# Performance work log

Hardware: AMD Instinct MI355X
Metric: run time of the kernel (lower is better)

Reference implementation:

```python
import jax, jax.numpy as jnp
import numpy as np

VOCAB, EMBED, CONV_C, HID, LABELS = 50257, 512, 512, 1024, 128
B, S = 32, 1024

def setup_inputs() -> dict:
    key = jax.random.key(0)
    ks = jax.random.split(key, 8)
    sc = lambda d: 1.0 / np.sqrt(d)
    return {
        "token_ids": jax.random.randint(ks[0], (B, S), 0, VOCAB),
        "emb_table": jax.random.normal(ks[1], (VOCAB, EMBED), jnp.float32) * 0.02,
        "conv_w": jax.random.normal(ks[2], (CONV_C, EMBED), jnp.float32) * sc(EMBED),
        "conv_b": jnp.zeros((CONV_C,), jnp.float32),
        "dec_w1": jax.random.normal(ks[3], (CONV_C, HID), jnp.float32) * sc(CONV_C),
        "dec_b1": jnp.zeros((HID,), jnp.float32),
        "dec_w2": jax.random.normal(ks[4], (HID, LABELS), jnp.float32) * sc(HID),
        "dec_b2": jnp.zeros((LABELS,), jnp.float32),
    }

def reference(token_ids, emb_table, conv_w, conv_b, dec_w1, dec_b1, dec_w2, dec_b2):
    # Embedding lookup: [B, S, E]
    x = emb_table[token_ids]
    # DocNN encoder on a length-1 sequence = kernel-1 conv + relu (+ trivial max-over-time)
    h = jax.nn.relu(jnp.einsum('bse,ce->bsc', x, conv_w) + conv_b)  # [B,S,C]
    # MLP decoder per word
    z = jax.nn.relu(jnp.einsum('bsc,ch->bsh', h, dec_w1) + dec_b1)  # [B,S,H]
    logits = jnp.einsum('bsh,hl->bsl', z, dec_w2) + dec_b2          # [B,S,L]
    # torch.cat over dim 0 of per-word outputs -> flat [B*S, L]
    return logits.reshape(-1, logits.shape[-1])
```

## Files before the change

kernel.cpp:

```cpp
#include <hip/hip_runtime.h>

typedef __bf16 bf16;
typedef __bf16 bf16x4 __attribute__((ext_vector_type(4)));
typedef __bf16 bf16x8 __attribute__((ext_vector_type(8)));
typedef float f32x4 __attribute__((ext_vector_type(4)));

#define NROWS 32768
#define EMBED 512
#define CONV_C 512
#define HID 1024
#define LABELS 128

__device__ inline void async16(const void* g, void* l) {
  __builtin_amdgcn_global_load_lds(
      (const __attribute__((address_space(1))) void*)g,
      (__attribute__((address_space(3))) void*)l, 16, 0, 0);
}

__device__ inline int bitswap02(int g) {
  return ((g & 1) << 2) | (g & 0xA) | ((g >> 2) & 1);
}

__device__ inline bf16x8 cvt8_sw(const float* row, int o0, int o1) {
  f32x4 lo = *(const f32x4*)(row + o0);
  f32x4 hi = *(const f32x4*)(row + o1);
  bf16x8 r;
  r[0] = (bf16)lo[0]; r[1] = (bf16)lo[1]; r[2] = (bf16)lo[2]; r[3] = (bf16)lo[3];
  r[4] = (bf16)hi[0]; r[5] = (bf16)hi[1]; r[6] = (bf16)hi[2]; r[7] = (bf16)hi[3];
  return r;
}


__global__ void cvt_bf16(const float* __restrict__ in, bf16* __restrict__ out, int n) {
  int i = (blockIdx.x * blockDim.x + threadIdx.x) * 4;
  if (i >= n) return;
  float4 v = *(const float4*)(in + i);
  bf16x4 o;
  o.x = (bf16)v.x; o.y = (bf16)v.y; o.z = (bf16)v.z; o.w = (bf16)v.w;
  *(bf16x4*)(out + i) = o;
}

__global__ void transpose_cvt(const float* __restrict__ in, bf16* __restrict__ out,
                              int K, int N) {
  __shared__ float t[64][65];
  int kb = blockIdx.x * 64, nb = blockIdx.y * 64;
  for (int i = threadIdx.x; i < 4096; i += 256) {
    int r = i >> 6, c = i & 63;
    t[r][c] = in[(size_t)(kb + r) * N + nb + c];
  }
  __syncthreads();
  for (int i = threadIdx.x; i < 4096; i += 256) {
    int r = i >> 6, c = i & 63;
    out[(size_t)(nb + r) * K + kb + c] = (bf16)t[c][r];
  }
}

__global__ __launch_bounds__(512, 2) void gemm1_gather(
    const int* __restrict__ tok, const float* __restrict__ emb,
    const bf16* __restrict__ convw, const float* __restrict__ bias,
    bf16* __restrict__ out, int M, int N, int K) {
  __shared__ __attribute__((aligned(16))) char smem[131072];
  const int tid = threadIdx.x, wave = tid >> 6, lane = tid & 63;
  const int m0 = blockIdx.x * 128;
  const int am0 = (wave >> 2) * 64;
  const int bn0 = (wave & 3) * 64;
  const int lrow = lane & 15, quad = lane >> 4;

  int a_r[4], a_c[4];
#pragma unroll
  for (int c = 0; c < 4; ++c) {
    int s = tid + c * 512;
    int r = s >> 4, p = s & 15;
    a_r[c] = r;
    a_c[c] = ((((p & 7) ^ (r & 7)) | (p & 8))) * 4;
  }
  int trow[4];
#pragma unroll
  for (int c = 0; c < 4; ++c) trow[c] = tok[m0 + a_r[c]];

  int b_r[4], b_c[4];
#pragma unroll
  for (int c = 0; c < 4; ++c) {
    int s = tid + c * 512;
    b_r[c] = s >> 3;
    b_c[c] = ((s & 7) ^ (b_r[c] & 7)) * 8;
  }

  auto stageA = [&](int p, int k0) {
    float* lAf = (float*)(smem + p * 32768);
#pragma unroll
    for (int c = 0; c < 4; ++c)
      async16(emb + (size_t)trow[c] * EMBED + k0 + a_c[c],
              lAf + (size_t)(tid + c * 512) * 4);
  };
  auto stageB = [&](int p, int cn0, int k0) {
    bf16* lB = (bf16*)(smem + 65536 + p * 32768);
#pragma unroll
    for (int c = 0; c < 4; ++c)
      async16(convw + (size_t)(cn0 + b_r[c]) * EMBED + k0 + b_c[c],
              lB + (size_t)(tid + c * 512) * 8);
  };

  const f32x4 zero4 = {0.f, 0.f, 0.f, 0.f};

  for (int chunk = 0; chunk < 2; ++chunk) {
    const int cn0 = chunk * 256;
    stageA(0, 0);
    stageB(0, cn0, 0);

    f32x4 acc[4][4];
#pragma unroll
    for (int i = 0; i < 4; ++i)
#pragma unroll
      for (int j = 0; j < 4; ++j) acc[i][j] = zero4;

    int cur = 0;
    for (int it = 0; it < 8; ++it) {
      __syncthreads();
      if (it < 7) {
        stageA(cur ^ 1, (it + 1) * 64);
        stageB(cur ^ 1, cn0, (it + 1) * 64);
      }
      const float* lAf = (const float*)(smem + cur * 32768);
      const bf16* lB = (const bf16*)(smem + 65536 + cur * 32768);
#pragma unroll
      for (int ks = 0; ks < 2; ++ks) {
        bf16x8 a[4], b[4];
#pragma unroll
        for (int t = 0; t < 4; ++t) {
          int r = am0 + t * 16 + lrow, sw = r & 7;
          int p0 = ks * 8 + ((2 * quad) ^ sw);
          int p1 = ks * 8 + ((2 * quad + 1) ^ sw);
          a[t] = cvt8_sw(lAf + r * 64, p0 * 4, p1 * 4);
        }
#pragma unroll
        for (int t = 0; t < 4; ++t) {
          int rn = bn0 + t * 16 + lrow;
          b[t] = *(const bf16x8*)(lB + rn * 64 + (((ks * 4 + quad) ^ (rn & 7)) * 8));
        }
#pragma unroll
        for (int mi = 0; mi < 4; ++mi)
#pragma unroll
          for (int ni = 0; ni < 4; ++ni)
            acc[mi][ni] =
                __builtin_amdgcn_mfma_f32_16x16x32_bf16(a[mi], b[ni], acc[mi][ni], 0, 0, 0);
      }
      cur ^= 1;
    }

#pragma unroll
    for (int mi = 0; mi < 4; ++mi) {
#pragma unroll
      for (int ni = 0; ni < 4; ++ni) {
        int col = cn0 + bn0 + ni * 16 + lrow;
        float bv = bias[col];
#pragma unroll
        for (int r = 0; r < 4; ++r) {
          int row = m0 + am0 + mi * 16 + quad * 4 + r;
          float v = acc[mi][ni][r] + bv;
          v = v > 0.f ? v : 0.f;
          out[(size_t)row * CONV_C + col] = (bf16)v;
        }
      }
    }
  }
}

__global__ __launch_bounds__(512, 2) void gemm23_fused(
    const bf16* __restrict__ h,
    const bf16* __restrict__ w1t,
    const bf16* __restrict__ w2t,
    const float* __restrict__ b1, const float* __restrict__ b2,
    float* __restrict__ out) {
  __shared__ __attribute__((aligned(16))) char smem[131072];
  bf16* zbuf = (bf16*)(smem + 32768);
  const int tid = threadIdx.x, wave = tid >> 6, lane = tid & 63;
  const int m0 = blockIdx.x * 128;
  const int am0 = (wave >> 2) * 64;
  const int bn0 = (wave & 3) * 64;
  const int lb0 = (wave & 3) * 32;
  const int lrow = lane & 15, quad = lane >> 4;
  const int lsw = lrow & 7;
  const int bsw = bitswap02(lsw);

  int a_r[2], a_c[2];
#pragma unroll
  for (int c = 0; c < 2; ++c) {
    int s = tid + c * 512;
    a_r[c] = s >> 3;
    a_c[c] = ((s & 7) ^ (a_r[c] & 7)) * 8;
  }
  int b_r[4], b_c[4];
#pragma unroll
  for (int c = 0; c < 4; ++c) {
    int s = tid + c * 512;
    b_r[c] = s >> 3;
    b_c[c] = ((s & 7) ^ (b_r[c] & 7)) * 8;
  }
  int q_r[2], q_c[2];
#pragma unroll
  for (int c = 0; c < 2; ++c) {
    int s = tid + c * 512;
    q_r[c] = s >> 3;
    q_c[c] = ((s & 7) ^ (q_r[c] & 7)) * 8;
  }

  auto stageA = [&](int p, int k0) {
    bf16* lA = (bf16*)(smem + p * 16384);
#pragma unroll
    for (int c = 0; c < 2; ++c)
      async16(h + (size_t)(m0 + a_r[c]) * 512 + k0 + a_c[c],
              lA + (size_t)(tid + c * 512) * 8);
  };
  auto stageB = [&](int p, int cn0, int k0) {
    bf16* lB = (bf16*)(smem + 32768 + p * 32768);
#pragma unroll
    for (int c = 0; c < 4; ++c)
      async16(w1t + (size_t)(cn0 + b_r[c]) * 512 + k0 + b_c[c],
              lB + (size_t)(tid + c * 512) * 8);
  };
  auto stageQ = [&](int cn0, int qq, int pq) {
    bf16* lQ = (bf16*)(smem + 98304 + pq * 16384);
#pragma unroll
    for (int c = 0; c < 2; ++c)
      async16(w2t + (size_t)q_r[c] * HID + cn0 + qq * 64 + q_c[c],
              lQ + (size_t)(tid + c * 512) * 8);
  };

  const f32x4 zero4 = {0.f, 0.f, 0.f, 0.f};
  f32x4 out_acc[4][2];
#pragma unroll
  for (int i = 0; i < 4; ++i)
#pragma unroll
    for (int j = 0; j < 2; ++j) out_acc[i][j] = zero4;

  auto layer3 = [&](int qq, int pq) {
    const bf16* lQ = (const bf16*)(smem + 98304 + pq * 16384);
#pragma unroll
    for (int ks = 0; ks < 2; ++ks) {
      bf16x8 a3[4], b3[2];
#pragma unroll
      for (int t = 0; t < 4; ++t) {
        int m = am0 + t * 16 + lrow;
        int kq = qq * 8 + ks * 4 + quad;
        a3[t] = *(const bf16x8*)(zbuf + m * 256 + ((kq ^ bsw) << 3));
      }
#pragma unroll
      for (int t = 0; t < 2; ++t) {
        int lab = lb0 + t * 16 + lrow;
        b3[t] = *(const bf16x8*)(lQ + lab * 64 + (((ks * 4 + quad) ^ lsw) * 8));
      }
#pragma unroll
      for (int mi = 0; mi < 4; ++mi)
#pragma unroll
        for (int ni = 0; ni < 2; ++ni)
          out_acc[mi][ni] =
              __builtin_amdgcn_mfma_f32_16x16x32_bf16(a3[mi], b3[ni], out_acc[mi][ni], 0, 0, 0);
    }
  };

  for (int chunk = 0; chunk < 4; ++chunk) {
    const int cn0 = chunk * 256;
    if (chunk == 0) stageA(0, 0);
    stageB(0, cn0, 0);
    stageQ(cn0, 0, 0);

    f32x4 z_acc[4][4];
#pragma unroll
    for (int i = 0; i < 4; ++i)
#pragma unroll
      for (int j = 0; j < 4; ++j) z_acc[i][j] = zero4;

    int cur = 0;
    for (int it = 0; it < 8; ++it) {
      __syncthreads();
      if (it < 7) {
        stageB(cur ^ 1, cn0, (it + 1) * 64);
        stageA(cur ^ 1, (it + 1) * 64);
      }
      const bf16* lA = (const bf16*)(smem + cur * 16384);
      const bf16* lB = (const bf16*)(smem + 32768 + cur * 32768);
#pragma unroll
      for (int ks = 0; ks < 2; ++ks) {
        bf16x8 a[4], b[4];
#pragma unroll
        for (int t = 0; t < 4; ++t)
          a[t] = *(const bf16x8*)(lA + (am0 + t * 16 + lrow) * 64 +
                                  (((ks * 4 + quad) ^ lsw) * 8));
#pragma unroll
        for (int t = 0; t < 4; ++t)
          b[t] = *(const bf16x8*)(lB + (bn0 + t * 16 + lrow) * 64 +
                                  (((ks * 4 + quad) ^ lsw) * 8));
#pragma unroll
        for (int mi = 0; mi < 4; ++mi)
#pragma unroll
          for (int ni = 0; ni < 4; ++ni)
            z_acc[mi][ni] =
                __builtin_amdgcn_mfma_f32_16x16x32_bf16(a[mi], b[ni], z_acc[mi][ni], 0, 0, 0);
      }
      cur ^= 1;
    }

    __syncthreads();
    stageQ(cn0, 1, 1);
#pragma unroll
    for (int mi = 0; mi < 4; ++mi) {
#pragma unroll
      for (int ni = 0; ni < 4; ++ni) {
        int zcol = bn0 + ni * 16 + lrow;
        float bv = b1[cn0 + zcol];
        int q5 = zcol >> 3;
#pragma unroll
        for (int r = 0; r < 4; ++r) {
          int zrow = am0 + mi * 16 + quad * 4 + r;
          float v = z_acc[mi][ni][r] + bv;
          v = v > 0.f ? v : 0.f;
          zbuf[zrow * 256 + ((q5 ^ bitswap02(zrow & 7)) << 3) + (zcol & 7)] = (bf16)v;
        }
      }
    }
    __syncthreads();
    layer3(0, 0);
    __syncthreads();
    stageQ(cn0, 2, 0);
    layer3(1, 1);
    __syncthreads();
    stageQ(cn0, 3, 1);
    if (chunk < 3) stageA(0, 0);
    layer3(2, 0);
    __syncthreads();
    layer3(3, 1);
    __syncthreads();
  }

#pragma unroll
  for (int mi = 0; mi < 4; ++mi) {
#pragma unroll
    for (int ni = 0; ni < 2; ++ni) {
      int col = lb0 + ni * 16 + lrow;
      float bv = b2[col];
#pragma unroll
      for (int r = 0; r < 4; ++r) {
        int row = m0 + am0 + mi * 16 + quad * 4 + r;
        out[(size_t)row * LABELS + col] = out_acc[mi][ni][r] + bv;
      }
    }
  }
}


extern "C" void kernel_launch(void* const* d_in, const int* in_sizes, int n_in,
                              void* d_out, int out_size, void* d_ws, size_t ws_size,
                              hipStream_t stream) {
  const int* tok = (const int*)d_in[0];
  const float* emb = (const float*)d_in[1];
  const float* conv_w = (const float*)d_in[2];
  const float* conv_b = (const float*)d_in[3];
  const float* w1 = (const float*)d_in[4];
  const float* b1 = (const float*)d_in[5];
  const float* w2 = (const float*)d_in[6];
  const float* b2 = (const float*)d_in[7];
  float* out = (float*)d_out;

  char* ws = (char*)d_ws;
  bf16* wtc = (bf16*)(ws);
  bf16* wt1 = (bf16*)(ws + (1u << 19));
  bf16* wt2 = (bf16*)(ws + 3 * (1u << 19));
  bf16* h = (bf16*)(ws + (2u << 20));

  hipLaunchKernelGGL(cvt_bf16, dim3(256), dim3(256), 0, stream,
                     conv_w, wtc, CONV_C * EMBED);
  hipLaunchKernelGGL(transpose_cvt, dim3(8, 16), dim3(256), 0, stream,
                     w1, wt1, CONV_C, HID);
  hipLaunchKernelGGL(transpose_cvt, dim3(16, 2), dim3(256), 0, stream,
                     w2, wt2, HID, LABELS);

  hipLaunchKernelGGL(gemm1_gather, dim3(NROWS / 128), dim3(512),
                     0, stream, tok, emb, wtc, conv_b, h, NROWS, CONV_C, EMBED);
  hipLaunchKernelGGL(gemm23_fused, dim3(NROWS / 128), dim3(512),
                     0, stream, h, wt1, wt2, b1, b2, out);
}
```

Measured before the change: 237.1 us.

## Switch both GEMM mainloops to 4-stage, 32-wide K pipelines with explicit vmcnt waits

Both the gather GEMM and the fused layer-2 GEMM drop their double-buffered 64-wide K tiles for a ring of four 32-wide K slices, issued three slices ahead. Waits use explicit s_waitcnt vmcnt counts and raw s_barrier with sched_barrier fences, and the MFMA block is raised in priority with s_setprio. This aims to hide global-to-LDS latency better and to cut the full __syncthreads drains. In exchange there are twice as many barriers per K step, and the hand-tuned vmcnt counts are fragile; a wrong count is a silent race.

```diff
diff --git a/kernel.cpp b/kernel.cpp
--- a/kernel.cpp
+++ b/kernel.cpp
@@ -10,6 +10,14 @@
 #define CONV_C 512
 #define HID 1024
 #define LABELS 128
+
+#define VMCNT(n) asm volatile("s_waitcnt vmcnt(" #n ")" ::: "memory")
+
+__device__ inline void sbar() {
+  __builtin_amdgcn_sched_barrier(0);
+  __builtin_amdgcn_s_barrier();
+  __builtin_amdgcn_sched_barrier(0);
+}
 
 __device__ inline void async16(const void* g, void* l) {
   __builtin_amdgcn_global_load_lds(
@@ -66,47 +74,46 @@
   const int bn0 = (wave & 3) * 64;
   const int lrow = lane & 15, quad = lane >> 4;
 
-  int a_r[4], a_c[4];
-#pragma unroll
-  for (int c = 0; c < 4; ++c) {
+  int a_r[2], a_c[2];
+#pragma unroll
+  for (int c = 0; c < 2; ++c) {
     int s = tid + c * 512;
-    int r = s >> 4, p = s & 15;
-    a_r[c] = r;
-    a_c[c] = ((((p & 7) ^ (r & 7)) | (p & 8))) * 4;
-  }
-  int trow[4];
-#pragma unroll
-  for (int c = 0; c < 4; ++c) trow[c] = tok[m0 + a_r[c]];
-
-  int b_r[4], b_c[4];
-#pragma unroll
-  for (int c = 0; c < 4; ++c) {
+    a_r[c] = s >> 3;
+    a_c[c] = ((s & 7) ^ (a_r[c] & 7)) * 4;
+  }
+  int trow[2];
+#pragma unroll
+  for (int c = 0; c < 2; ++c) trow[c] = tok[m0 + a_r[c]];
+
+  int b_r[2], b_c[2];
+#pragma unroll
+  for (int c = 0; c < 2; ++c) {
     int s = tid + c * 512;
-    b_r[c] = s >> 3;
-    b_c[c] = ((s & 7) ^ (b_r[c] & 7)) * 8;
-  }
-
-  auto stageA = [&](int p, int k0) {
-    float* lAf = (float*)(smem + p * 32768);
-#pragma unroll
-    for (int c = 0; c < 4; ++c)
-      async16(emb + (size_t)trow[c] * EMBED + k0 + a_c[c],
-              lAf + (size_t)(tid + c * 512) * 4);
-  };
-  auto stageB = [&](int p, int cn0, int k0) {
-    bf16* lB = (bf16*)(smem + 65536 + p * 32768);
-#pragma unroll
-    for (int c = 0; c < 4; ++c)
-      async16(convw + (size_t)(cn0 + b_r[c]) * EMBED + k0 + b_c[c],
-              lB + (size_t)(tid + c * 512) * 8);
-  };
+    b_r[c] = s >> 2;
+    b_c[c] = ((s & 3) ^ (b_r[c] & 3)) * 8;
+  }
+
+  const int pA0 = (2 * quad) ^ (lrow & 7);
+  const int fswB = (quad ^ (lrow & 3)) << 3;
 
   const f32x4 zero4 = {0.f, 0.f, 0.f, 0.f};
 
   for (int chunk = 0; chunk < 2; ++chunk) {
     const int cn0 = chunk * 256;
-    stageA(0, 0);
-    stageB(0, cn0, 0);
+
+    auto stage_half = [&](int hh) {
+      const int sl = hh & 3, k0 = hh * 32;
+      float* lAf = (float*)(smem + sl * 16384);
+#pragma unroll
+      for (int c = 0; c < 2; ++c)
+        async16(emb + (size_t)trow[c] * EMBED + k0 + a_c[c],
+                lAf + (size_t)(tid + c * 512) * 4);
+      bf16* lB = (bf16*)(smem + 65536 + sl * 16384);
+#pragma unroll
+      for (int c = 0; c < 2; ++c)
+        async16(convw + (size_t)(cn0 + b_r[c]) * EMBED + k0 + b_c[c],
+                lB + (size_t)(tid + c * 512) * 8);
+    };
 
     f32x4 acc[4][4];
 #pragma unroll
@@ -114,38 +121,40 @@
 #pragma unroll
       for (int j = 0; j < 4; ++j) acc[i][j] = zero4;
 
-    int cur = 0;
-    for (int it = 0; it < 8; ++it) {
-      __syncthreads();
-      if (it < 7) {
-        stageA(cur ^ 1, (it + 1) * 64);
-        stageB(cur ^ 1, cn0, (it + 1) * 64);
-      }
-      const float* lAf = (const float*)(smem + cur * 32768);
-      const bf16* lB = (const bf16*)(smem + 65536 + cur * 32768);
-#pragma unroll
-      for (int ks = 0; ks < 2; ++ks) {
-        bf16x8 a[4], b[4];
-#pragma unroll
-        for (int t = 0; t < 4; ++t) {
-          int r = am0 + t * 16 + lrow, sw = r & 7;
-          int p0 = ks * 8 + ((2 * quad) ^ sw);
-          int p1 = ks * 8 + ((2 * quad + 1) ^ sw);
-          a[t] = cvt8_sw(lAf + r * 64, p0 * 4, p1 * 4);
-        }
-#pragma unroll
-        for (int t = 0; t < 4; ++t) {
-          int rn = bn0 + t * 16 + lrow;
-          b[t] = *(const bf16x8*)(lB + rn * 64 + (((ks * 4 + quad) ^ (rn & 7)) * 8));
-        }
-#pragma unroll
-        for (int mi = 0; mi < 4; ++mi)
-#pragma unroll
-          for (int ni = 0; ni < 4; ++ni)
-            acc[mi][ni] =
-                __builtin_amdgcn_mfma_f32_16x16x32_bf16(a[mi], b[ni], acc[mi][ni], 0, 0, 0);
-      }
-      cur ^= 1;
+    __builtin_amdgcn_sched_barrier(0);
+    stage_half(0); stage_half(1); stage_half(2);
+    VMCNT(8);
+    sbar();
+
+#pragma unroll
+    for (int hh = 0; hh < 16; ++hh) {
+      const float* lAf = (const float*)(smem + (hh & 3) * 16384);
+      const bf16* lB = (const bf16*)(smem + 65536 + (hh & 3) * 16384);
+      bf16x8 a[4], b[4];
+#pragma unroll
+      for (int t = 0; t < 4; ++t) {
+        int r = am0 + t * 16 + lrow;
+        a[t] = cvt8_sw(lAf + r * 32, pA0 * 4, (pA0 ^ 1) * 4);
+      }
+#pragma unroll
+      for (int t = 0; t < 4; ++t) {
+        int r = bn0 + t * 16 + lrow;
+        b[t] = *(const bf16x8*)(lB + r * 32 + fswB);
+      }
+      if (hh + 3 < 16) stage_half(hh + 3);
+      if (hh <= 12) { VMCNT(8); }
+      else if (hh == 13) { VMCNT(4); }
+      else { VMCNT(0); }
+      sbar();
+      __builtin_amdgcn_s_setprio(1);
+#pragma unroll
+      for (int mi = 0; mi < 4; ++mi)
+#pragma unroll
+        for (int ni = 0; ni < 4; ++ni)
+          acc[mi][ni] =
+              __builtin_amdgcn_mfma_f32_16x16x32_bf16(a[mi], b[ni], acc[mi][ni], 0, 0, 0);
+      __builtin_amdgcn_s_setprio(0);
+      sbar();
     }
 
 #pragma unroll
@@ -183,19 +192,14 @@
   const int lsw = lrow & 7;
   const int bsw = bitswap02(lsw);
 
-  int a_r[2], a_c[2];
+  const int a_r = tid >> 2;
+  const int a_c = ((tid & 3) ^ (a_r & 3)) * 8;
+  int b_r[2], b_c[2];
 #pragma unroll
   for (int c = 0; c < 2; ++c) {
     int s = tid + c * 512;
-    a_r[c] = s >> 3;
-    a_c[c] = ((s & 7) ^ (a_r[c] & 7)) * 8;
-  }
-  int b_r[4], b_c[4];
-#pragma unroll
-  for (int c = 0; c < 4; ++c) {
-    int s = tid + c * 512;
-    b_r[c] = s >> 3;
-    b_c[c] = ((s & 7) ^ (b_r[c] & 7)) * 8;
+    b_r[c] = s >> 2;
+    b_c[c] = ((s & 3) ^ (b_r[c] & 3)) * 8;
   }
   int q_r[2], q_c[2];
 #pragma unroll
@@ -205,20 +209,8 @@
     q_c[c] = ((s & 7) ^ (q_r[c] & 7)) * 8;
   }
 
-  auto stageA = [&](int p, int k0) {
-    bf16* lA = (bf16*)(smem + p * 16384);
-#pragma unroll
-    for (int c = 0; c < 2; ++c)
-      async16(h + (size_t)(m0 + a_r[c]) * 512 + k0 + a_c[c],
-              lA + (size_t)(tid + c * 512) * 8);
-  };
-  auto stageB = [&](int p, int cn0, int k0) {
-    bf16* lB = (bf16*)(smem + 32768 + p * 32768);
-#pragma unroll
-    for (int c = 0; c < 4; ++c)
-      async16(w1t + (size_t)(cn0 + b_r[c]) * 512 + k0 + b_c[c],
-              lB + (size_t)(tid + c * 512) * 8);
-  };
+  const int fsw = (quad ^ (lrow & 3)) << 3;
+
   auto stageQ = [&](int cn0, int qq, int pq) {
     bf16* lQ = (bf16*)(smem + 98304 + pq * 16384);
 #pragma unroll
@@ -261,47 +253,62 @@
 
   for (int chunk = 0; chunk < 4; ++chunk) {
     const int cn0 = chunk * 256;
-    if (chunk == 0) stageA(0, 0);
-    stageB(0, cn0, 0);
+
+    auto stage_half = [&](int hh) {
+      const int sl = hh & 3, k0 = hh * 32;
+      bf16* lA = (bf16*)(smem + sl * 8192);
+      async16(h + (size_t)(m0 + a_r) * 512 + k0 + a_c, lA + (size_t)tid * 8);
+      bf16* lB = (bf16*)(smem + 32768 + sl * 16384);
+#pragma unroll
+      for (int c = 0; c < 2; ++c)
+        async16(w1t + (size_t)(cn0 + b_r[c]) * 512 + k0 + b_c[c],
+                lB + (size_t)(tid + c * 512) * 8);
+    };
+
+    f32x4 z_acc[4][4];
+#pragma unroll
+    for (int i = 0; i < 4; ++i)
+#pragma unroll
+      for (int j = 0; j < 4; ++j) z_acc[i][j] = zero4;
+
+    __builtin_amdgcn_sched_barrier(0);
+    stage_half(0); stage_half(1); stage_half(2);
     stageQ(cn0, 0, 0);
-
-    f32x4 z_acc[4][4];
-#pragma unroll
-    for (int i = 0; i < 4; ++i)
-#pragma unroll
-      for (int j = 0; j < 4; ++j) z_acc[i][j] = zero4;
-
-    int cur = 0;
-    for (int it = 0; it < 8; ++it) {
-      __syncthreads();
-      if (it < 7) {
-        stageB(cur ^ 1, cn0, (it + 1) * 64);
-        stageA(cur ^ 1, (it + 1) * 64);
-      }
-      const bf16* lA = (const bf16*)(smem + cur * 16384);
-      const bf16* lB = (const bf16*)(smem + 32768 + cur * 32768);
-#pragma unroll
-      for (int ks = 0; ks < 2; ++ks) {
-        bf16x8 a[4], b[4];
-#pragma unroll
-        for (int t = 0; t < 4; ++t)
-          a[t] = *(const bf16x8*)(lA + (am0 + t * 16 + lrow) * 64 +
-                                  (((ks * 4 + quad) ^ lsw) * 8));
-#pragma unroll
-        for (int t = 0; t < 4; ++t)
-          b[t] = *(const bf16x8*)(lB + (bn0 + t * 16 + lrow) * 64 +
-                                  (((ks * 4 + quad) ^ lsw) * 8));
-#pragma unroll
-        for (int mi = 0; mi < 4; ++mi)
-#pragma unroll
-          for (int ni = 0; ni < 4; ++ni)
-            z_acc[mi][ni] =
-                __builtin_amdgcn_mfma_f32_16x16x32_bf16(a[mi], b[ni], z_acc[mi][ni], 0, 0, 0);
-      }
-      cur ^= 1;
-    }
-
-    __syncthreads();
+    VMCNT(8);
+    sbar();
+
+#pragma unroll
+    for (int hh = 0; hh < 16; ++hh) {
+      const bf16* lA = (const bf16*)(smem + (hh & 3) * 8192);
+      const bf16* lB = (const bf16*)(smem + 32768 + (hh & 3) * 16384);
+      bf16x8 a[4], b[4];
+#pragma unroll
+      for (int t = 0; t < 4; ++t) {
+        int r = am0 + t * 16 + lrow;
+        a[t] = *(const bf16x8*)(lA + r * 32 + fsw);
+      }
+#pragma unroll
+      for (int t = 0; t < 4; ++t) {
+        int r = bn0 + t * 16 + lrow;
+        b[t] = *(const bf16x8*)(lB + r * 32 + fsw);
+      }
+      if (hh + 3 < 16) stage_half(hh + 3);
+      if (hh <= 1) { VMCNT(8); }
+      else if (hh <= 12) { VMCNT(6); }
+      else if (hh == 13) { VMCNT(3); }
+      else { VMCNT(0); }
+      sbar();
+      __builtin_amdgcn_s_setprio(1);
+#pragma unroll
+      for (int mi = 0; mi < 4; ++mi)
+#pragma unroll
+        for (int ni = 0; ni < 4; ++ni)
+          z_acc[mi][ni] =
+              __builtin_amdgcn_mfma_f32_16x16x32_bf16(a[mi], b[ni], z_acc[mi][ni], 0, 0, 0);
+      __builtin_amdgcn_s_setprio(0);
+      sbar();
+    }
+
     stageQ(cn0, 1, 1);
 #pragma unroll
     for (int mi = 0; mi < 4; ++mi) {
@@ -326,7 +333,6 @@
     layer3(1, 1);
     __syncthreads();
     stageQ(cn0, 3, 1);
-    if (chunk < 3) stageA(0, 0);
     layer3(2, 0);
     __syncthreads();
     layer3(3, 1);
```

Result: slower. 242.5 us (+2.3%).

## Triple-buffer A tiles and use counted vmcnt waits with raw barriers in layer-2 loop

Applied to the files above, without the earlier changes.

The layer-2 K loop in the fused GEMM now keeps three LDS buffers for the activation tile and two for the weight tile. It replaces __syncthreads with an explicit s_waitcnt vmcnt(2) and a raw s_barrier, so global-to-LDS prefetches for later iterations stay in flight across the barrier. The W2 tile staging moves after the loop, and the A prefetch that used to overlap layer 3 is now issued at each chunk start. This raises LDS use to 144KB per block. The correctness of the hand-counted vmcnt values depends on exactly how many loads each stage issues.

```diff
diff --git a/kernel.cpp b/kernel.cpp
--- a/kernel.cpp
+++ b/kernel.cpp
@@ -10,6 +10,14 @@
 #define CONV_C 512
 #define HID 1024
 #define LABELS 128
+
+#define VMCNT(n) asm volatile("s_waitcnt vmcnt(" #n ")" ::: "memory")
+
+__device__ inline void sbar() {
+  __builtin_amdgcn_sched_barrier(0);
+  __builtin_amdgcn_s_barrier();
+  __builtin_amdgcn_sched_barrier(0);
+}
 
 __device__ inline void async16(const void* g, void* l) {
   __builtin_amdgcn_global_load_lds(
@@ -172,8 +180,8 @@
     const bf16* __restrict__ w2t,
     const float* __restrict__ b1, const float* __restrict__ b2,
     float* __restrict__ out) {
-  __shared__ __attribute__((aligned(16))) char smem[131072];
-  bf16* zbuf = (bf16*)(smem + 32768);
+  __shared__ __attribute__((aligned(16))) char smem[147456];
+  bf16* zbuf = (bf16*)(smem + 49152);
   const int tid = threadIdx.x, wave = tid >> 6, lane = tid & 63;
   const int m0 = blockIdx.x * 128;
   const int am0 = (wave >> 2) * 64;
@@ -213,14 +221,14 @@
               lA + (size_t)(tid + c * 512) * 8);
   };
   auto stageB = [&](int p, int cn0, int k0) {
-    bf16* lB = (bf16*)(smem + 32768 + p * 32768);
+    bf16* lB = (bf16*)(smem + 49152 + p * 32768);
 #pragma unroll
     for (int c = 0; c < 4; ++c)
       async16(w1t + (size_t)(cn0 + b_r[c]) * 512 + k0 + b_c[c],
               lB + (size_t)(tid + c * 512) * 8);
   };
   auto stageQ = [&](int cn0, int qq, int pq) {
-    bf16* lQ = (bf16*)(smem + 98304 + pq * 16384);
+    bf16* lQ = (bf16*)(smem + 114688 + pq * 16384);
 #pragma unroll
     for (int c = 0; c < 2; ++c)
       async16(w2t + (size_t)q_r[c] * HID + cn0 + qq * 64 + q_c[c],
@@ -235,7 +243,7 @@
     for (int j = 0; j < 2; ++j) out_acc[i][j] = zero4;
 
   auto layer3 = [&](int qq, int pq) {
-    const bf16* lQ = (const bf16*)(smem + 98304 + pq * 16384);
+    const bf16* lQ = (const bf16*)(smem + 114688 + pq * 16384);
 #pragma unroll
     for (int ks = 0; ks < 2; ++ks) {
       bf16x8 a3[4], b3[2];
@@ -261,9 +269,10 @@
 
   for (int chunk = 0; chunk < 4; ++chunk) {
     const int cn0 = chunk * 256;
-    if (chunk == 0) stageA(0, 0);
+
     stageB(0, cn0, 0);
-    stageQ(cn0, 0, 0);
+    stageA(0, 0);
+    stageA(1, 64);
 
     f32x4 z_acc[4][4];
 #pragma unroll
@@ -271,26 +280,27 @@
 #pragma unroll
       for (int j = 0; j < 4; ++j) z_acc[i][j] = zero4;
 
-    int cur = 0;
+#pragma unroll
     for (int it = 0; it < 8; ++it) {
-      __syncthreads();
-      if (it < 7) {
-        stageB(cur ^ 1, cn0, (it + 1) * 64);
-        stageA(cur ^ 1, (it + 1) * 64);
-      }
-      const bf16* lA = (const bf16*)(smem + cur * 16384);
-      const bf16* lB = (const bf16*)(smem + 32768 + cur * 32768);
+      if (it < 7) { VMCNT(2); } else { VMCNT(0); }
+      sbar();
+      if (it < 7) stageB((it + 1) & 1, cn0, (it + 1) * 64);
+      if (it < 6) stageA((it + 2) % 3, (it + 2) * 64);
+      const bf16* lA = (const bf16*)(smem + (it % 3) * 16384);
+      const bf16* lB = (const bf16*)(smem + 49152 + (it & 1) * 32768);
 #pragma unroll
       for (int ks = 0; ks < 2; ++ks) {
         bf16x8 a[4], b[4];
 #pragma unroll
-        for (int t = 0; t < 4; ++t)
-          a[t] = *(const bf16x8*)(lA + (am0 + t * 16 + lrow) * 64 +
-                                  (((ks * 4 + quad) ^ lsw) * 8));
-#pragma unroll
-        for (int t = 0; t < 4; ++t)
-          b[t] = *(const bf16x8*)(lB + (bn0 + t * 16 + lrow) * 64 +
-                                  (((ks * 4 + quad) ^ lsw) * 8));
+        for (int t = 0; t < 4; ++t) {
+          int r = am0 + t * 16 + lrow;
+          a[t] = *(const bf16x8*)(lA + r * 64 + (((ks * 4 + quad) ^ (r & 7)) * 8));
+        }
+#pragma unroll
+        for (int t = 0; t < 4; ++t) {
+          int r = bn0 + t * 16 + lrow;
+          b[t] = *(const bf16x8*)(lB + r * 64 + (((ks * 4 + quad) ^ (r & 7)) * 8));
+        }
 #pragma unroll
         for (int mi = 0; mi < 4; ++mi)
 #pragma unroll
@@ -298,10 +308,10 @@
             z_acc[mi][ni] =
                 __builtin_amdgcn_mfma_f32_16x16x32_bf16(a[mi], b[ni], z_acc[mi][ni], 0, 0, 0);
       }
-      cur ^= 1;
-    }
-
-    __syncthreads();
+    }
+    sbar();
+
+    stageQ(cn0, 0, 0);
     stageQ(cn0, 1, 1);
 #pragma unroll
     for (int mi = 0; mi < 4; ++mi) {
@@ -326,7 +336,6 @@
     layer3(1, 1);
     __syncthreads();
     stageQ(cn0, 3, 1);
-    if (chunk < 3) stageA(0, 0);
     layer3(2, 0);
     __syncthreads();
     layer3(3, 1);
```

Measured after the change: 245.2 us. 1.03x slower.
